# Optimization experiments

Measured on AMD Instinct MI355X. Metric: run time of the kernel, lower is better.

Reference implementation:

```python
import jax, jax.numpy as jnp
import numpy as np

E, H, KV, D = 2048, 32, 8, 64  # embed_dim, n_head, n_kv_head, head_dim
B, C = 1, 2048
G = H // KV  # GQA group size = 4


def setup_inputs() -> dict:
    key = jax.random.key(0)
    k0, k1, k2, k3, k4 = jax.random.split(key, 5)
    s = 0.02
    return {
        "x": jax.random.normal(k0, (B, C, E), dtype=jnp.float32),
        "W_q": jax.random.normal(k1, (H * D, E), dtype=jnp.float32) * s,
        "W_k": jax.random.normal(k2, (KV * D, E), dtype=jnp.float32) * s,
        "W_v": jax.random.normal(k3, (KV * D, E), dtype=jnp.float32) * s,
        "W_o": jax.random.normal(k4, (E, H * D), dtype=jnp.float32) * s,
    }


def reference(x, W_q, W_k, W_v, W_o):
    b, c, e = x.shape
    # bias-free projections (nn.Linear applies x @ W.T)
    Q = (x @ W_q.T).reshape(b, c, KV, G, D)   # [B,C,KV,G,D]
    K = (x @ W_k.T).reshape(b, c, KV, D)      # [B,C,KV,D]
    V = (x @ W_v.T).reshape(b, c, KV, D)
    scale = 1.0 / jnp.sqrt(jnp.float32(D))
    # grouped-query attention scores: query heads grouped per KV head
    scores = jnp.einsum("bqkgd,bskd->bkgqs", Q, K) * scale  # [B,KV,G,Cq,Cs]
    causal = jnp.tril(jnp.ones((c, c), dtype=bool))
    scores = jnp.where(causal, scores, jnp.finfo(scores.dtype).min)
    attn = jax.nn.softmax(scores, axis=-1)
    hidden = jnp.einsum("bkgqs,bskd->bqkgd", attn, V)  # [B,Cq,KV,G,D]
    hidden = hidden.reshape(b, c, H * D)
    return hidden @ W_o.T
```

## Files before the change

kernel.cpp:

```cpp
#include <hip/hip_runtime.h>
#include <stdint.h>
#include <stddef.h>

#define CLEN 2048
#define EMB  2048
#define NH   32
#define NKV  8
#define HD   64

#define SZ_X  (CLEN * EMB)
#define SZ_WQ (NH * HD * EMB)
#define SZ_WK (NKV * HD * EMB)
#define SZ_WV (NKV * HD * EMB)
#define SZ_WO (EMB * NH * HD)
#define SZ_ALL (SZ_X + SZ_WQ + SZ_WK + SZ_WV + SZ_WO)

typedef __attribute__((ext_vector_type(8))) short short8v;
typedef __attribute__((ext_vector_type(4))) short short4v;
typedef __attribute__((ext_vector_type(4))) float float4v;

#define MFMA16(A, B, C) __builtin_amdgcn_mfma_f32_16x16x32_bf16((A), (B), (C), 0, 0, 0)

__device__ __forceinline__ uint16_t f2bf(float f) {
  union { float f; unsigned int u; } c;
  c.f = f;
  return (uint16_t)((c.u + 0x7fffu + ((c.u >> 16) & 1u)) >> 16);
}

__device__ __forceinline__ void gload_lds16(const uint16_t* g, uint16_t* l) {
  __builtin_amdgcn_global_load_lds((const __attribute__((address_space(1))) void*)g,
                                   (__attribute__((address_space(3))) void*)l, 16, 0, 0);
}

__global__ __launch_bounds__(256) void cvt_all(
    const float* __restrict__ s0, const float* __restrict__ s1,
    const float* __restrict__ s2, const float* __restrict__ s3,
    const float* __restrict__ s4, uint16_t* __restrict__ dst)
{
  const long i = ((long)blockIdx.x * 256 + threadIdx.x) * 4;
  if (i >= SZ_ALL) return;
  const float* src;
  long off;
  if (i < SZ_X)                         { src = s0; off = i; }
  else if (i < SZ_X + SZ_WQ)            { src = s1; off = i - SZ_X; }
  else if (i < SZ_X + SZ_WQ + SZ_WK)    { src = s2; off = i - (SZ_X + SZ_WQ); }
  else if (i < SZ_X + SZ_WQ + SZ_WK + SZ_WV) { src = s3; off = i - (SZ_X + SZ_WQ + SZ_WK); }
  else                                  { src = s4; off = i - (SZ_X + SZ_WQ + SZ_WK + SZ_WV); }
  const float4v v = *(const float4v*)(src + off);
  short4v p;
#pragma unroll
  for (int j = 0; j < 4; ++j) p[j] = (short)f2bf(v[j]);
  *(short4v*)(dst + i) = p;
}

template <int OMODE>
__device__ __forceinline__ void gemm_body8(
    const uint16_t* __restrict__ A, const uint16_t* __restrict__ B,
    uint16_t* __restrict__ Co, float* __restrict__ Cf,
    int m0, int n0, int M, int N, int Kd)
{
  __shared__ uint16_t As[128 * 32];
  __shared__ uint16_t Bs[128 * 32];
  const int tid = threadIdx.x;
  const int w = tid >> 6, l = tid & 63;
  const int wr = (w >> 1) << 5;
  const int wc = (w & 1) << 6;
  const int lr = l & 15, lhi = l >> 4;

  float4v acc[2][4] = {};

  const int rL = tid >> 2;
  const int kL = (tid & 3) << 3;
  const uint16_t* Ag = A + (size_t)(m0 + rL) * Kd + kL;
  const uint16_t* Bg = B + (size_t)(n0 + rL) * Kd + kL;
  uint16_t* AsW = As + w * 512;
  uint16_t* BsW = Bs + w * 512;

  for (int k0 = 0; k0 < Kd; k0 += 32) {
    __syncthreads();
    gload_lds16(Ag + k0, AsW);
    gload_lds16(Bg + k0, BsW);
    __syncthreads();

    short8v a[2], b[4];
#pragma unroll
    for (int i = 0; i < 2; ++i)
      a[i] = *(const short8v*)(As + (wr + i * 16 + lr) * 32 + lhi * 8);
#pragma unroll
    for (int j = 0; j < 4; ++j)
      b[j] = *(const short8v*)(Bs + (wc + j * 16 + lr) * 32 + lhi * 8);
#pragma unroll
    for (int i = 0; i < 2; ++i)
#pragma unroll
      for (int j = 0; j < 4; ++j)
        acc[i][j] = MFMA16(a[i], b[j], acc[i][j]);
  }

  if (OMODE == 1) {
#pragma unroll
    for (int i = 0; i < 2; ++i) {
      const int m = m0 + wr + i * 16 + lhi * 4;
#pragma unroll
      for (int j = 0; j < 4; ++j) {
        const int n = n0 + wc + j * 16 + lr;
        short4v pk;
#pragma unroll
        for (int r = 0; r < 4; ++r) pk[r] = (short)f2bf(acc[i][j][r]);
        *(short4v*)(Co + (size_t)n * M + m) = pk;
      }
    }
  } else if (OMODE == 0) {
#pragma unroll
    for (int i = 0; i < 2; ++i) {
      const int m = m0 + wr + i * 16 + lhi * 4;
#pragma unroll
      for (int j = 0; j < 4; ++j) {
        const int n = n0 + wc + j * 16 + lr;
#pragma unroll
        for (int r = 0; r < 4; ++r)
          Co[(size_t)(m + r) * N + n] = f2bf(acc[i][j][r]);
      }
    }
  } else {
#pragma unroll
    for (int i = 0; i < 2; ++i) {
      const int m = m0 + wr + i * 16 + lhi * 4;
#pragma unroll
      for (int j = 0; j < 4; ++j) {
        const int n = n0 + wc + j * 16 + lr;
#pragma unroll
        for (int r = 0; r < 4; ++r)
          Cf[(size_t)(m + r) * N + n] = acc[i][j][r];
      }
    }
  }
}

__global__ __launch_bounds__(512) void qkv_gemm(
    const uint16_t* __restrict__ x,
    const uint16_t* __restrict__ Wq, const uint16_t* __restrict__ Wk,
    const uint16_t* __restrict__ Wv,
    uint16_t* __restrict__ Qw, uint16_t* __restrict__ Kw, uint16_t* __restrict__ Vtw)
{
  const int m0 = blockIdx.x << 7;
  const int bn = blockIdx.y;
  if (bn < 16) {
    gemm_body8<0>(x, Wq, Qw, nullptr, m0, bn << 7, CLEN, NH * HD, EMB);
  } else if (bn < 20) {
    gemm_body8<0>(x, Wk, Kw, nullptr, m0, (bn - 16) << 7, CLEN, NKV * HD, EMB);
  } else {
    gemm_body8<1>(x, Wv, Vtw, nullptr, m0, (bn - 20) << 7, CLEN, NKV * HD, EMB);
  }
}

__global__ __launch_bounds__(512) void out_gemm(
    const uint16_t* __restrict__ Hh, const uint16_t* __restrict__ Wo,
    float* __restrict__ out)
{
  gemm_body8<2>(Hh, Wo, nullptr, out, blockIdx.x << 7, blockIdx.y << 7, CLEN, EMB, NH * HD);
}

#define SCL 0.1803368801111244f

__global__ __launch_bounds__(256) void attn_fwd(
    const uint16_t* __restrict__ Q, const uint16_t* __restrict__ Kx,
    const uint16_t* __restrict__ Vt, uint16_t* __restrict__ Hd)
{
  const int h = blockIdx.y;
  const int x = blockIdx.x;
  const int kvh = h >> 2;
  const int tid = threadIdx.x, w = tid >> 6, l = tid & 63;
  const int lr = l & 15, lhi = l >> 4;

  __shared__ uint16_t Ks[2][64 * 64];
  __shared__ uint16_t Vs[2][64 * 64];
  __shared__ uint16_t Pl[4][16 * 72];

  short8v ones;
#pragma unroll
  for (int c = 0; c < 8; ++c) ones[c] = (short)0x3F80;

  const int sr8 = l >> 3;
  const int scol = (((l & 7) ^ sr8) << 3);

  for (int it = 0; it < 2; ++it) {
    const int qt = it ? (31 - x) : x;
    const int q0 = qt << 6;

    short8v qf[2];
    {
      const uint16_t* qp = Q + (size_t)(q0 + w * 16 + lr) * (NH * HD) + h * HD + lhi * 8;
      qf[0] = *(const short8v*)qp;
      qf[1] = *(const short8v*)(qp + 32);
    }

    float4v o[4] = {};
    float4v osum = {};

    const int ntile = qt + 1;

#pragma unroll
    for (int i = 0; i < 2; ++i) {
      const int c = (i << 2) | w;
      const int srow = (c << 3) | sr8;
      gload_lds16(Kx + (size_t)srow * (NKV * HD) + kvh * HD + scol, Ks[0] + c * 512);
      gload_lds16(Vt + (size_t)(kvh * HD + srow) * CLEN + scol,     Vs[0] + c * 512);
    }
    __syncthreads();

    int cur = 0;
    for (int s = 0; s < ntile; ++s) {
      if (s + 1 < ntile) {
        const int kv1 = (s + 1) << 6;
#pragma unroll
        for (int i = 0; i < 2; ++i) {
          const int c = (i << 2) | w;
          const int srow = (c << 3) | sr8;
          gload_lds16(Kx + (size_t)(kv1 + srow) * (NKV * HD) + kvh * HD + scol,
                      Ks[cur ^ 1] + c * 512);
          gload_lds16(Vt + (size_t)(kvh * HD + srow) * CLEN + kv1 + scol,
                      Vs[cur ^ 1] + c * 512);
        }
      }

      const char* KsB = (const char*)Ks[cur];
      const char* VsB = (const char*)Vs[cur];

      float4v sf[4];
      __builtin_amdgcn_s_setprio(1);
#pragma unroll
      for (int nb = 0; nb < 4; ++nb) {
        const int row = nb * 16 + lr;
        const int rowb = row * 128, sw = (row & 7) << 4;
        float4v a0 = {};
        a0 = MFMA16(qf[0], *(const short8v*)(KsB + ((rowb + lhi * 16) ^ sw)), a0);
        a0 = MFMA16(qf[1], *(const short8v*)(KsB + ((rowb + 64 + lhi * 16) ^ sw)), a0);
        sf[nb] = a0;
      }
      __builtin_amdgcn_s_setprio(0);

      if (s == ntile - 1) {
        const int qbase = q0 + w * 16 + lhi * 4;
        const int kbase = s * 64 + lr;
#pragma unroll
        for (int nb = 0; nb < 4; ++nb)
#pragma unroll
          for (int r = 0; r < 4; ++r) {
            float vv = sf[nb][r] * SCL;
            vv = (kbase + nb * 16 <= qbase + r) ? vv : -3e38f;
            sf[nb][r] = __builtin_amdgcn_exp2f(vv);
          }
      } else {
#pragma unroll
        for (int nb = 0; nb < 4; ++nb)
#pragma unroll
          for (int r = 0; r < 4; ++r)
            sf[nb][r] = __builtin_amdgcn_exp2f(sf[nb][r] * SCL);
      }

#pragma unroll
      for (int nb = 0; nb < 4; ++nb)
#pragma unroll
        for (int r = 0; r < 4; ++r)
          Pl[w][(lhi * 4 + r) * 72 + nb * 16 + lr] = f2bf(sf[nb][r]);
      const short8v pf0 = *(const short8v*)&Pl[w][lr * 72 + lhi * 8];
      const short8v pf1 = *(const short8v*)&Pl[w][lr * 72 + 32 + lhi * 8];

      __builtin_amdgcn_s_setprio(1);
#pragma unroll
      for (int j = 0; j < 4; ++j) {
        const int row = j * 16 + lr;
        const int rowb = row * 128, sw = (row & 7) << 4;
        o[j] = MFMA16(pf0, *(const short8v*)(VsB + ((rowb + lhi * 16) ^ sw)), o[j]);
        o[j] = MFMA16(pf1, *(const short8v*)(VsB + ((rowb + 64 + lhi * 16) ^ sw)), o[j]);
      }
      osum = MFMA16(pf0, ones, osum);
      osum = MFMA16(pf1, ones, osum);
      __builtin_amdgcn_s_setprio(0);

      __syncthreads();
      cur ^= 1;
    }

#pragma unroll
    for (int r = 0; r < 4; ++r) {
      const float inv = 1.0f / osum[r];
      const size_t qq = (size_t)(q0 + w * 16 + lhi * 4 + r);
#pragma unroll
      for (int j = 0; j < 4; ++j)
        Hd[qq * (NH * HD) + h * HD + j * 16 + lr] = f2bf(o[j][r] * inv);
    }
  }
}

extern "C" void kernel_launch(void* const* d_in, const int* in_sizes, int n_in,
                              void* d_out, int out_size, void* d_ws, size_t ws_size,
                              hipStream_t stream) {
  const float* x  = (const float*)d_in[0];
  const float* Wq = (const float*)d_in[1];
  const float* Wk = (const float*)d_in[2];
  const float* Wv = (const float*)d_in[3];
  const float* Wo = (const float*)d_in[4];

  uint16_t* ws  = (uint16_t*)d_ws;
  uint16_t* xb  = ws;
  uint16_t* Wqb = xb  + SZ_X;
  uint16_t* Wkb = Wqb + SZ_WQ;
  uint16_t* Wvb = Wkb + SZ_WK;
  uint16_t* Wob = Wvb + SZ_WV;
  uint16_t* Qw  = Wob + SZ_WO;
  uint16_t* Kw  = Qw  + (size_t)CLEN * (NH * HD);
  uint16_t* Vtw = Kw  + (size_t)CLEN * (NKV * HD);
  uint16_t* Hw  = Vtw + (size_t)CLEN * (NKV * HD);

  cvt_all<<<SZ_ALL / 1024, 256, 0, stream>>>(x, Wq, Wk, Wv, Wo, ws);
  qkv_gemm<<<dim3(16, 24), 512, 0, stream>>>(xb, Wqb, Wkb, Wvb, Qw, Kw, Vtw);
  attn_fwd<<<dim3(16, 32), 256, 0, stream>>>(Qw, Kw, Vtw, Hw);
  out_gemm<<<dim3(16, 16), 512, 0, stream>>>(Hw, Wob, (float*)d_out);
}
```

Measured before the change: 140.5 us.

## Load K and V fragments directly from global into registers, dropping LDS staging

The attention kernel no longer stages K and V tiles through double-buffered shared memory with block-wide barriers. Each wave loads its own K and V MFMA operands straight from global memory into registers, prefetching the next K tile in a ping-pong register pair and unrolling the loop by two. This removes the LDS traffic and the per-tile __syncthreads. In exchange, every wave re-reads the same K/V data from global memory (4x redundant traffic per block, served from cache), register pressure rises, and V loads are not prefetched ahead of use.

```diff
diff --git a/kernel.cpp b/kernel.cpp
--- a/kernel.cpp
+++ b/kernel.cpp
@@ -172,26 +172,24 @@
   const int tid = threadIdx.x, w = tid >> 6, l = tid & 63;
   const int lr = l & 15, lhi = l >> 4;
 
-  __shared__ uint16_t Ks[2][64 * 64];
-  __shared__ uint16_t Vs[2][64 * 64];
   __shared__ uint16_t Pl[4][16 * 72];
 
   short8v ones;
 #pragma unroll
   for (int c = 0; c < 8; ++c) ones[c] = (short)0x3F80;
 
-  const int sr8 = l >> 3;
-  const int scol = (((l & 7) ^ sr8) << 3);
+  const uint16_t* Kp = Kx + (size_t)lr * (NKV * HD) + kvh * HD + lhi * 8;
+  const uint16_t* Vp = Vt + (size_t)(kvh * HD + lr) * CLEN + lhi * 8;
 
   for (int it = 0; it < 2; ++it) {
     const int qt = it ? (31 - x) : x;
     const int q0 = qt << 6;
 
-    short8v qf[2];
+    short8v qf0, qf1;
     {
       const uint16_t* qp = Q + (size_t)(q0 + w * 16 + lr) * (NH * HD) + h * HD + lhi * 8;
-      qf[0] = *(const short8v*)qp;
-      qf[1] = *(const short8v*)(qp + 32);
+      qf0 = *(const short8v*)qp;
+      qf1 = *(const short8v*)(qp + 32);
     }
 
     float4v o[4] = {};
@@ -199,49 +197,49 @@
 
     const int ntile = qt + 1;
 
-#pragma unroll
-    for (int i = 0; i < 2; ++i) {
-      const int c = (i << 2) | w;
-      const int srow = (c << 3) | sr8;
-      gload_lds16(Kx + (size_t)srow * (NKV * HD) + kvh * HD + scol, Ks[0] + c * 512);
-      gload_lds16(Vt + (size_t)(kvh * HD + srow) * CLEN + scol,     Vs[0] + c * 512);
-    }
-    __syncthreads();
-
-    int cur = 0;
-    for (int s = 0; s < ntile; ++s) {
+    short8v kA[4][2], kB[4][2];
+
+#pragma unroll
+    for (int nb = 0; nb < 4; ++nb) {
+      const uint16_t* kp = Kp + (size_t)(nb * 16) * (NKV * HD);
+      kA[nb][0] = *(const short8v*)kp;
+      kA[nb][1] = *(const short8v*)(kp + 32);
+    }
+
+    auto body = [&](int s, short8v (&kc)[4][2], short8v (&kn)[4][2]) {
+      const int kv0 = s << 6;
+
+      short8v vf[4][2];
+#pragma unroll
+      for (int j = 0; j < 4; ++j) {
+        const uint16_t* vp = Vp + (size_t)(j * 16) * CLEN + kv0;
+        vf[j][0] = *(const short8v*)vp;
+        vf[j][1] = *(const short8v*)(vp + 32);
+      }
       if (s + 1 < ntile) {
-        const int kv1 = (s + 1) << 6;
-#pragma unroll
-        for (int i = 0; i < 2; ++i) {
-          const int c = (i << 2) | w;
-          const int srow = (c << 3) | sr8;
-          gload_lds16(Kx + (size_t)(kv1 + srow) * (NKV * HD) + kvh * HD + scol,
-                      Ks[cur ^ 1] + c * 512);
-          gload_lds16(Vt + (size_t)(kvh * HD + srow) * CLEN + kv1 + scol,
-                      Vs[cur ^ 1] + c * 512);
+        const int kv1 = kv0 + 64;
+#pragma unroll
+        for (int nb = 0; nb < 4; ++nb) {
+          const uint16_t* kp = Kp + (size_t)(kv1 + nb * 16) * (NKV * HD);
+          kn[nb][0] = *(const short8v*)kp;
+          kn[nb][1] = *(const short8v*)(kp + 32);
         }
       }
-
-      const char* KsB = (const char*)Ks[cur];
-      const char* VsB = (const char*)Vs[cur];
 
       float4v sf[4];
       __builtin_amdgcn_s_setprio(1);
 #pragma unroll
       for (int nb = 0; nb < 4; ++nb) {
-        const int row = nb * 16 + lr;
-        const int rowb = row * 128, sw = (row & 7) << 4;
         float4v a0 = {};
-        a0 = MFMA16(qf[0], *(const short8v*)(KsB + ((rowb + lhi * 16) ^ sw)), a0);
-        a0 = MFMA16(qf[1], *(const short8v*)(KsB + ((rowb + 64 + lhi * 16) ^ sw)), a0);
+        a0 = MFMA16(qf0, kc[nb][0], a0);
+        a0 = MFMA16(qf1, kc[nb][1], a0);
         sf[nb] = a0;
       }
       __builtin_amdgcn_s_setprio(0);
 
       if (s == ntile - 1) {
         const int qbase = q0 + w * 16 + lhi * 4;
-        const int kbase = s * 64 + lr;
+        const int kbase = kv0 + lr;
 #pragma unroll
         for (int nb = 0; nb < 4; ++nb)
 #pragma unroll
@@ -269,17 +267,17 @@
       __builtin_amdgcn_s_setprio(1);
 #pragma unroll
       for (int j = 0; j < 4; ++j) {
-        const int row = j * 16 + lr;
-        const int rowb = row * 128, sw = (row & 7) << 4;
-        o[j] = MFMA16(pf0, *(const short8v*)(VsB + ((rowb + lhi * 16) ^ sw)), o[j]);
-        o[j] = MFMA16(pf1, *(const short8v*)(VsB + ((rowb + 64 + lhi * 16) ^ sw)), o[j]);
+        o[j] = MFMA16(pf0, vf[j][0], o[j]);
+        o[j] = MFMA16(pf1, vf[j][1], o[j]);
       }
       osum = MFMA16(pf0, ones, osum);
       osum = MFMA16(pf1, ones, osum);
       __builtin_amdgcn_s_setprio(0);
-
-      __syncthreads();
-      cur ^= 1;
+    };
+
+    for (int s = 0; s < ntile; s += 2) {
+      body(s, kA, kB);
+      if (s + 1 < ntile) body(s + 1, kB, kA);
     }
 
 #pragma unroll
```

After: 218.5 us. 1.55x slower.

## Use BK=64 swizzled LDS tiles and narrower N tiles for KV and output GEMMs

Applied to the files above, without the earlier changes.

The GEMM body now loads K-slices of 64 instead of 32 into XOR-swizzled shared memory, which halves the number of barrier-synchronized iterations and is meant to avoid LDS bank conflicts. The N tile width is templated: Q projection keeps 128-wide tiles, while K/V and output projections use 64-wide tiles, so those launches get more blocks (grids grow to 16x32) for better CU occupancy. The cost is more LDS per block and re-reading A for the narrower tiles. The attention kernel changes are cosmetic.

```diff
diff --git a/kernel.cpp b/kernel.cpp
--- a/kernel.cpp
+++ b/kernel.cpp
@@ -53,47 +53,57 @@
   *(short4v*)(dst + i) = p;
 }
 
-template <int OMODE>
-__device__ __forceinline__ void gemm_body8(
+template <int NW, int OMODE>
+__device__ __forceinline__ void gemm_bk64(
     const uint16_t* __restrict__ A, const uint16_t* __restrict__ B,
     uint16_t* __restrict__ Co, float* __restrict__ Cf,
     int m0, int n0, int M, int N, int Kd)
 {
-  __shared__ uint16_t As[128 * 32];
-  __shared__ uint16_t Bs[128 * 32];
+  __shared__ uint16_t As[128 * 64];
+  __shared__ uint16_t Bs[32 * NW * 64];
   const int tid = threadIdx.x;
   const int w = tid >> 6, l = tid & 63;
   const int wr = (w >> 1) << 5;
-  const int wc = (w & 1) << 6;
+  const int wc = (w & 1) * (NW << 4);
   const int lr = l & 15, lhi = l >> 4;
-
-  float4v acc[2][4] = {};
-
-  const int rL = tid >> 2;
-  const int kL = (tid & 3) << 3;
-  const uint16_t* Ag = A + (size_t)(m0 + rL) * Kd + kL;
-  const uint16_t* Bg = B + (size_t)(n0 + rL) * Kd + kL;
-  uint16_t* AsW = As + w * 512;
-  uint16_t* BsW = Bs + w * 512;
-
-  for (int k0 = 0; k0 < Kd; k0 += 32) {
+  const int swz = (lr & 7) << 4;
+
+  float4v acc[2][NW] = {};
+
+  const int sr8 = l >> 3;
+  const int scol = (((l & 7) ^ sr8) << 3);
+
+  for (int k0 = 0; k0 < Kd; k0 += 64) {
     __syncthreads();
-    gload_lds16(Ag + k0, AsW);
-    gload_lds16(Bg + k0, BsW);
+    gload_lds16(A + (size_t)(m0 + (w << 3) + sr8) * Kd + k0 + scol,       As + w * 512);
+    gload_lds16(A + (size_t)(m0 + ((w + 8) << 3) + sr8) * Kd + k0 + scol, As + (w + 8) * 512);
+    gload_lds16(B + (size_t)(n0 + (w << 3) + sr8) * Kd + k0 + scol,       Bs + w * 512);
+    if (NW == 4)
+      gload_lds16(B + (size_t)(n0 + ((w + 8) << 3) + sr8) * Kd + k0 + scol, Bs + (w + 8) * 512);
     __syncthreads();
 
-    short8v a[2], b[4];
-#pragma unroll
-    for (int i = 0; i < 2; ++i)
-      a[i] = *(const short8v*)(As + (wr + i * 16 + lr) * 32 + lhi * 8);
-#pragma unroll
-    for (int j = 0; j < 4; ++j)
-      b[j] = *(const short8v*)(Bs + (wc + j * 16 + lr) * 32 + lhi * 8);
-#pragma unroll
-    for (int i = 0; i < 2; ++i)
-#pragma unroll
-      for (int j = 0; j < 4; ++j)
-        acc[i][j] = MFMA16(a[i], b[j], acc[i][j]);
+    short8v a[2][2], b[NW][2];
+#pragma unroll
+    for (int i = 0; i < 2; ++i) {
+      const int row = wr + i * 16 + lr;
+#pragma unroll
+      for (int ks = 0; ks < 2; ++ks)
+        a[i][ks] = *(const short8v*)((const char*)As + row * 128 + ((ks * 64 + lhi * 16) ^ swz));
+    }
+#pragma unroll
+    for (int j = 0; j < NW; ++j) {
+      const int row = wc + j * 16 + lr;
+#pragma unroll
+      for (int ks = 0; ks < 2; ++ks)
+        b[j][ks] = *(const short8v*)((const char*)Bs + row * 128 + ((ks * 64 + lhi * 16) ^ swz));
+    }
+#pragma unroll
+    for (int ks = 0; ks < 2; ++ks)
+#pragma unroll
+      for (int i = 0; i < 2; ++i)
+#pragma unroll
+        for (int j = 0; j < NW; ++j)
+          acc[i][j] = MFMA16(a[i][ks], b[j][ks], acc[i][j]);
   }
 
   if (OMODE == 1) {
@@ -101,7 +111,7 @@
     for (int i = 0; i < 2; ++i) {
       const int m = m0 + wr + i * 16 + lhi * 4;
 #pragma unroll
-      for (int j = 0; j < 4; ++j) {
+      for (int j = 0; j < NW; ++j) {
         const int n = n0 + wc + j * 16 + lr;
         short4v pk;
 #pragma unroll
@@ -114,7 +124,7 @@
     for (int i = 0; i < 2; ++i) {
       const int m = m0 + wr + i * 16 + lhi * 4;
 #pragma unroll
-      for (int j = 0; j < 4; ++j) {
+      for (int j = 0; j < NW; ++j) {
         const int n = n0 + wc + j * 16 + lr;
 #pragma unroll
         for (int r = 0; r < 4; ++r)
@@ -126,7 +136,7 @@
     for (int i = 0; i < 2; ++i) {
       const int m = m0 + wr + i * 16 + lhi * 4;
 #pragma unroll
-      for (int j = 0; j < 4; ++j) {
+      for (int j = 0; j < NW; ++j) {
         const int n = n0 + wc + j * 16 + lr;
 #pragma unroll
         for (int r = 0; r < 4; ++r)
@@ -145,11 +155,11 @@
   const int m0 = blockIdx.x << 7;
   const int bn = blockIdx.y;
   if (bn < 16) {
-    gemm_body8<0>(x, Wq, Qw, nullptr, m0, bn << 7, CLEN, NH * HD, EMB);
-  } else if (bn < 20) {
-    gemm_body8<0>(x, Wk, Kw, nullptr, m0, (bn - 16) << 7, CLEN, NKV * HD, EMB);
+    gemm_bk64<4, 0>(x, Wq, Qw, nullptr, m0, bn << 7, CLEN, NH * HD, EMB);
+  } else if (bn < 24) {
+    gemm_bk64<2, 0>(x, Wk, Kw, nullptr, m0, (bn - 16) << 6, CLEN, NKV * HD, EMB);
   } else {
-    gemm_body8<1>(x, Wv, Vtw, nullptr, m0, (bn - 20) << 7, CLEN, NKV * HD, EMB);
+    gemm_bk64<2, 1>(x, Wv, Vtw, nullptr, m0, (bn - 24) << 6, CLEN, NKV * HD, EMB);
   }
 }
 
@@ -157,7 +167,7 @@
     const uint16_t* __restrict__ Hh, const uint16_t* __restrict__ Wo,
     float* __restrict__ out)
 {
-  gemm_body8<2>(Hh, Wo, nullptr, out, blockIdx.x << 7, blockIdx.y << 7, CLEN, EMB, NH * HD);
+  gemm_bk64<2, 2>(Hh, Wo, nullptr, out, blockIdx.x << 7, blockIdx.y << 6, CLEN, EMB, NH * HD);
 }
 
 #define SCL 0.1803368801111244f
@@ -187,11 +197,11 @@
     const int qt = it ? (31 - x) : x;
     const int q0 = qt << 6;
 
-    short8v qf[2];
+    short8v qf0, qf1;
     {
       const uint16_t* qp = Q + (size_t)(q0 + w * 16 + lr) * (NH * HD) + h * HD + lhi * 8;
-      qf[0] = *(const short8v*)qp;
-      qf[1] = *(const short8v*)(qp + 32);
+      qf0 = *(const short8v*)qp;
+      qf1 = *(const short8v*)(qp + 32);
     }
 
     float4v o[4] = {};
@@ -233,15 +243,15 @@
         const int row = nb * 16 + lr;
         const int rowb = row * 128, sw = (row & 7) << 4;
         float4v a0 = {};
-        a0 = MFMA16(qf[0], *(const short8v*)(KsB + ((rowb + lhi * 16) ^ sw)), a0);
-        a0 = MFMA16(qf[1], *(const short8v*)(KsB + ((rowb + 64 + lhi * 16) ^ sw)), a0);
+        a0 = MFMA16(qf0, *(const short8v*)(KsB + ((rowb + lhi * 16) ^ sw)), a0);
+        a0 = MFMA16(qf1, *(const short8v*)(KsB + ((rowb + 64 + lhi * 16) ^ sw)), a0);
         sf[nb] = a0;
       }
       __builtin_amdgcn_s_setprio(0);
 
       if (s == ntile - 1) {
         const int qbase = q0 + w * 16 + lhi * 4;
-        const int kbase = s * 64 + lr;
+        const int kbase = (s << 6) + lr;
 #pragma unroll
         for (int nb = 0; nb < 4; ++nb)
 #pragma unroll
@@ -314,7 +324,7 @@
   uint16_t* Hw  = Vtw + (size_t)CLEN * (NKV * HD);
 
   cvt_all<<<SZ_ALL / 1024, 256, 0, stream>>>(x, Wq, Wk, Wv, Wo, ws);
-  qkv_gemm<<<dim3(16, 24), 512, 0, stream>>>(xb, Wqb, Wkb, Wvb, Qw, Kw, Vtw);
+  qkv_gemm<<<dim3(16, 32), 512, 0, stream>>>(xb, Wqb, Wkb, Wvb, Qw, Kw, Vtw);
   attn_fwd<<<dim3(16, 32), 256, 0, stream>>>(Qw, Kw, Vtw, Hw);
-  out_gemm<<<dim3(16, 16), 512, 0, stream>>>(Hw, Wob, (float*)d_out);
-}
+  out_gemm<<<dim3(16, 32), 512, 0, stream>>>(Hw, Wob, (float*)d_out);
+}
```

Measured after the change: 116.2 us. -17.3%, faster.
